# Kernel optimization log

Measured on AMD Instinct MI355X. Metric: run time of the kernel, lower is better.

## Reference

```python
import jax, jax.numpy as jnp
import numpy as np
from jax import lax

B = 4096
PRO_VOCAB, PRO_LEN, PRO_K = 25, 1000, 8
LIG_VOCAB, LIG_LEN, LIG_K = 64, 100, 4
CH = 96  # 2*CH = 192 = 6*32 per the reshape in the original forward
DN = ('NCH', 'OIH', 'NCH')  # 1D conv dimension numbers


def setup_inputs() -> dict:
    key = jax.random.key(0)
    ks = jax.random.split(key, 8)
    protein = jax.random.normal(ks[0], (B, PRO_VOCAB, PRO_LEN), dtype=jnp.float32)
    ligand = jax.random.normal(ks[1], (B, LIG_VOCAB, LIG_LEN), dtype=jnp.float32)
    w_pro = jax.random.normal(ks[2], (CH, PRO_VOCAB, PRO_K), dtype=jnp.float32) * 0.05
    b_pro = jnp.zeros((CH,), dtype=jnp.float32)
    w_lig = jax.random.normal(ks[3], (CH, LIG_VOCAB, LIG_K), dtype=jnp.float32) * 0.05
    b_lig = jnp.zeros((CH,), dtype=jnp.float32)
    # QuLinear readout over the 32*32=1024 amplitude-encoded Gram matrix -> scalar
    w_aff = jax.random.normal(ks[4], (1024,), dtype=jnp.float32) * 0.05
    b_aff = jnp.zeros((), dtype=jnp.float32)
    return {"protein": protein, "ligand": ligand, "w_pro": w_pro, "b_pro": b_pro,
            "w_lig": w_lig, "b_lig": b_lig, "w_aff": w_aff, "b_aff": b_aff}


def _conv_branch(x, w, b):
    # Conv1d (valid) -> ReLU -> global max pool over length  =>  (B, CH)
    y = lax.conv_general_dilated(x, w, (1,), 'VALID', dimension_numbers=DN)
    return jnp.max(jax.nn.relu(y + b[None, :, None]), axis=-1)


def reference(protein, ligand, w_pro, b_pro, w_lig, b_lig, w_aff, b_aff):
    x1 = _conv_branch(ligand, w_lig, b_lig)    # (B, 96)
    x2 = _conv_branch(protein, w_pro, b_pro)   # (B, 96)
    x = jnp.concatenate([x1, x2], axis=1).reshape(-1, 6, 32)  # (B, 6, 32)
    # Vectorized per-sample Gram matrix a.T @ a : (B, 32, 32)
    gram = jnp.einsum('bij,bik->bjk', x, x)
    flat = gram.reshape(gram.shape[0], -1)     # (B, 1024)
    # Amplitude encoding: L2-normalize the flattened Gram matrix per sample
    amp = flat / (jnp.linalg.norm(flat, axis=1, keepdims=True) + 1e-12)
    # QuLinear readout -> scalar affinity per sample
    aff = amp @ w_aff + b_aff                  # (B,)
    return aff
```

## Files before the change

kernel.cpp:

```cpp
#include <hip/hip_runtime.h>
#include <math.h>

typedef _Float16 f16;
typedef _Float16 f16x2 __attribute__((ext_vector_type(2)));
typedef _Float16 f16x4 __attribute__((ext_vector_type(4)));
typedef _Float16 f16x8 __attribute__((ext_vector_type(8)));
typedef float f32x4 __attribute__((ext_vector_type(4)));
typedef float f32x16 __attribute__((ext_vector_type(16)));

template<int V, int K, int VP>
__global__ void repack_kernel(const float* __restrict__ w, f16* __restrict__ wp) {
    int i = blockIdx.x * 256 + threadIdx.x;
    if (i >= K * 96 * VP) return;
    int v = i % VP, ch = (i / VP) % 96, t = i / (VP * 96);
    float val = (v < V) ? w[(ch * V + v) * K + t] : 0.f;
    wp[i] = (f16)val;
}

__global__ __launch_bounds__(256, 2) void conv_pro_kernel(
    const float* __restrict__ in,
    const f16*   __restrict__ wp,
    const float* __restrict__ bias,
    float* __restrict__ feat,
    int feat_off)
{
    constexpr int V = 25, L = 1000, KT = 8, LOUT = 993;
    constexpr int CH  = 256;
    constexpr int NC  = 4;
    constexpr int BR  = 264;
    constexpr int RSB = 80;
    constexpr int P4  = BR / 4;
    constexpr int NVP = 13;
    constexpr int NU  = NVP * P4;
    constexpr int NW  = KT * 96 * 32;

    __shared__ __align__(16) char s_raw[BR * RSB];
    __shared__ __align__(16) f16  s_w[NW];
    __shared__ float s_red[4 * 96];

    const int tid  = threadIdx.x;
    const int wave = tid >> 6;
    const int lane = tid & 63;
    const int g    = lane >> 4;
    const int r16  = lane & 15;
    const size_t b = blockIdx.x;
    const float* gs = in + b * (size_t)(V * L);

    {
        const f16x8* wg = (const f16x8*)wp;
        f16x8* wl = (f16x8*)s_w;
        #pragma unroll
        for (int u = 0; u < NW / 8 / 256; ++u)
            wl[u * 256 + tid] = wg[u * 256 + tid];
    }
    for (int row = tid; row < BR; row += 256) {
        const int swz = ((row >> 3) & 3) << 4;
        *(f16x8*)(s_raw + row * RSB + (48 ^ swz)) = (f16x8){};
    }
    __syncthreads();

    float runmax[6];
    #pragma unroll
    for (int c6 = 0; c6 < 6; ++c6) runmax[c6] = -3.0e38f;

    for (int c = 0; c < NC; ++c) {
        if (c) __syncthreads();
        #pragma unroll
        for (int u = 0; u < 4; ++u) {
            const int i = u * 256 + tid;
            if (i < NU) {
                const int v2 = i / P4, p4 = i - v2 * P4;
                const int p  = 4 * p4;
                const int gp = c * CH + p;
                float4 x0 = {0.f, 0.f, 0.f, 0.f}, x1 = {0.f, 0.f, 0.f, 0.f};
                if (gp < L) {
                    x0 = *(const float4*)(gs + (size_t)(2 * v2) * L + gp);
                    if (2 * v2 + 1 < V)
                        x1 = *(const float4*)(gs + (size_t)(2 * v2 + 1) * L + gp);
                }
                const int pb = 4 * v2;
                const int slot = pb & 48, sub = pb & 12;
                const float vx0[4] = {x0.x, x0.y, x0.z, x0.w};
                const float vx1[4] = {x1.x, x1.y, x1.z, x1.w};
                #pragma unroll
                for (int j = 0; j < 4; ++j) {
                    const int row = p + j;
                    const int swz = ((row >> 3) & 3) << 4;
                    f16x2 hv = { (f16)vx0[j], (f16)vx1[j] };
                    *(f16x2*)(s_raw + row * RSB + ((slot ^ swz) + sub)) = hv;
                }
            }
        }
        __syncthreads();

        f32x4 acc[4][6] = {};
        #pragma unroll 1
        for (int t = 0; t < KT; ++t) {
            f16x8 bf[6];
            #pragma unroll
            for (int c6 = 0; c6 < 6; ++c6)
                bf[c6] = *(const f16x8*)(s_w + (t * 96 + c6 * 16 + r16) * 32 + g * 8);
            #pragma unroll
            for (int rt = 0; rt < 4; ++rt) {
                const int row = wave * 64 + rt * 16 + r16 + t;
                const int swz = ((row >> 3) & 3) << 4;
                f16x8 a = *(const f16x8*)(s_raw + row * RSB + ((g * 16) ^ swz));
                #pragma unroll
                for (int c6 = 0; c6 < 6; ++c6)
                    acc[rt][c6] = __builtin_amdgcn_mfma_f32_16x16x32_f16(a, bf[c6], acc[rt][c6], 0, 0, 0);
            }
        }
        #pragma unroll
        for (int rt = 0; rt < 4; ++rt) {
            const int pt = c * CH + wave * 64 + rt * 16;
            if (pt + 16 <= LOUT) {
                #pragma unroll
                for (int c6 = 0; c6 < 6; ++c6)
                    #pragma unroll
                    for (int i = 0; i < 4; ++i)
                        runmax[c6] = fmaxf(runmax[c6], acc[rt][c6][i]);
            } else {
                const int p0g = pt + g * 4;
                #pragma unroll
                for (int c6 = 0; c6 < 6; ++c6)
                    #pragma unroll
                    for (int i = 0; i < 4; ++i)
                        if (p0g + i < LOUT) runmax[c6] = fmaxf(runmax[c6], acc[rt][c6][i]);
            }
        }
    }

    #pragma unroll
    for (int c6 = 0; c6 < 6; ++c6) {
        runmax[c6] = fmaxf(runmax[c6], __shfl_xor(runmax[c6], 16, 64));
        runmax[c6] = fmaxf(runmax[c6], __shfl_xor(runmax[c6], 32, 64));
    }
    if (lane < 16) {
        #pragma unroll
        for (int c6 = 0; c6 < 6; ++c6)
            s_red[wave * 96 + c6 * 16 + lane] = runmax[c6];
    }
    __syncthreads();
    if (tid < 96) {
        float m = fmaxf(fmaxf(s_red[tid], s_red[96 + tid]),
                        fmaxf(s_red[192 + tid], s_red[288 + tid]));
        feat[b * 192 + feat_off + tid] = fmaxf(m + bias[tid], 0.f);
    }
}

__global__ __launch_bounds__(384) void conv_lig_kernel(
    const float* __restrict__ in,
    const f16*   __restrict__ wp,
    const float* __restrict__ bias,
    float* __restrict__ feat,
    int feat_off)
{
    constexpr int V = 64, L = 100, KT = 4, VP = 64, KSTEPS = 4;
    constexpr int LP = 132, RS = 72, NTILES = 4, LOUT = 97;
    constexpr int RSB = RS * 2, NQ = V / 4;
    __shared__ __align__(16) char s_raw[LP * RSB];

    const int tid  = threadIdx.x;
    const int b    = blockIdx.x;
    const int wave = tid >> 6;
    const int lane = tid & 63;
    const int colw = wave % 3;
    const int roww = wave / 3;
    const int q    = lane >> 5;
    const int r    = lane & 31;

    {
        float4 z = {0.f, 0.f, 0.f, 0.f};
        float4* sz = (float4*)s_raw;
        for (int i = tid; i < LP * RSB / 16; i += 384) sz[i] = z;
    }
    __syncthreads();

    const float* gin = in + (size_t)b * (V * L);
    for (int i = tid; i < NQ * L; i += 384) {
        int q4 = i / L, p = i - q4 * L;
        const float* gp = gin + q4 * 4 * L + p;
        f16x4 hv = { (f16)gp[0], (f16)gp[L], (f16)gp[2 * L], (f16)gp[3 * L] };
        int off = (8 * q4) ^ (((p >> 3) & 3) << 4);
        *(f16x4*)(s_raw + p * RSB + off) = hv;
    }

    f16x8 bfr[KT][KSTEPS];
    #pragma unroll
    for (int t = 0; t < KT; ++t)
        #pragma unroll
        for (int ks = 0; ks < KSTEPS; ++ks)
            bfr[t][ks] = *(const f16x8*)(wp + (t * 96 + colw * 32 + r) * VP + ks * 16 + q * 8);

    __syncthreads();

    float runmax = -3.0e38f;
    for (int it = 0; it < NTILES / 2; ++it) {
        const int p0 = (roww * (NTILES / 2) + it) * 32;
        f32x16 acc = {};
        #pragma unroll
        for (int t = 0; t < KT; ++t) {
            int row = p0 + r + t;
            if (row > LP - 1) row = LP - 1;
            const char* ap = s_raw + row * RSB;
            const int swz = ((row >> 3) & 3) << 4;
            #pragma unroll
            for (int ks = 0; ks < KSTEPS; ++ks) {
                f16x8 af = *(const f16x8*)(ap + ((ks * 32 + q * 16) ^ swz));
                acc = __builtin_amdgcn_mfma_f32_32x32x16_f16(af, bfr[t][ks], acc, 0, 0, 0);
            }
        }
        #pragma unroll
        for (int i = 0; i < 16; ++i) {
            int rr = (i & 3) + 8 * (i >> 2) + 4 * q;
            if (p0 + rr < LOUT) runmax = fmaxf(runmax, acc[i]);
        }
    }
    runmax = fmaxf(runmax, __shfl_xor(runmax, 32, 64));

    __syncthreads();
    float* s_red = (float*)s_raw;
    if (lane < 32) s_red[roww * 96 + colw * 32 + r] = runmax;
    __syncthreads();
    if (tid < 96) {
        float m = fmaxf(s_red[tid], s_red[96 + tid]);
        feat[(size_t)b * 192 + feat_off + tid] = fmaxf(m + bias[tid], 0.f);
    }
}

__global__ __launch_bounds__(256) void gram_affinity_kernel(
    const float* __restrict__ feat, const float* __restrict__ w_aff,
    const float* __restrict__ b_aff, float* __restrict__ out, int B)
{
    const int lane = threadIdx.x & 63;
    const int wid  = threadIdx.x >> 6;
    const int b    = blockIdx.x * 4 + wid;

    __shared__ float s_x[4][192];

    if (b < B) {
        const float* fp = feat + (size_t)b * 192;
        for (int i = lane; i < 192; i += 64) s_x[wid][i] = fp[i];
    }
    __syncthreads();

    if (b < B) {
        float ssum = 0.f, sdot = 0.f;
        #pragma unroll
        for (int t = 0; t < 16; ++t) {
            const int jk = t * 64 + lane;
            const int j = jk >> 5, k = jk & 31;
            float gg = 0.f;
            #pragma unroll
            for (int i = 0; i < 6; ++i)
                gg = fmaf(s_x[wid][i * 32 + j], s_x[wid][i * 32 + k], gg);
            ssum = fmaf(gg, gg, ssum);
            sdot = fmaf(gg, w_aff[jk], sdot);
        }
        #pragma unroll
        for (int off = 32; off >= 1; off >>= 1) {
            ssum += __shfl_xor(ssum, off, 64);
            sdot += __shfl_xor(sdot, off, 64);
        }
        if (lane == 0) out[b] = sdot / (sqrtf(ssum) + 1e-12f) + b_aff[0];
    }
}

extern "C" void kernel_launch(void* const* d_in, const int* in_sizes, int n_in,
                              void* d_out, int out_size, void* d_ws, size_t ws_size,
                              hipStream_t stream)
{
    const float* protein = (const float*)d_in[0];
    const float* ligand  = (const float*)d_in[1];
    const float* w_pro   = (const float*)d_in[2];
    const float* b_pro   = (const float*)d_in[3];
    const float* w_lig   = (const float*)d_in[4];
    const float* b_lig   = (const float*)d_in[5];
    const float* w_aff   = (const float*)d_in[6];
    const float* b_aff   = (const float*)d_in[7];
    float* out = (float*)d_out;
    const int B = out_size;

    float* feat   = (float*)d_ws;
    f16*   wpackP = (f16*)((char*)d_ws + (size_t)B * 192 * 4);
    f16*   wpackL = wpackP + 8 * 96 * 32;

    repack_kernel<25, 8, 32><<<96, 256, 0, stream>>>(w_pro, wpackP);
    repack_kernel<64, 4, 64><<<96, 256, 0, stream>>>(w_lig, wpackL);

    conv_lig_kernel<<<B, 384, 0, stream>>>(ligand, wpackL, b_lig, feat, 0);
    conv_pro_kernel<<<B, 256, 0, stream>>>(protein, wpackP, b_pro, feat, 96);

    gram_affinity_kernel<<<(B + 3) / 4, 256, 0, stream>>>(feat, w_aff, b_aff, out, B);
}
```

Baseline: 304.2 us.

## Fuse Gram affinity readout into protein conv kernel with double-buffered 512-thread staging

The protein conv kernel now runs 512 threads per sample, processes the sequence in two 512-row chunks with double-buffered LDS, and overlaps staging of the second chunk with MFMA compute on the first. Staging writes 8 channels per 16-byte store using a new XOR swizzle. The Gram matrix plus normalized readout is folded into the kernel's epilogue, which removes the separate gram kernel launch and the feature round trip. The cost is larger LDS use (about 83 KB, one block per CU) and a serialized epilogue inside each block.

```diff
diff --git a/kernel.cpp b/kernel.cpp
--- a/kernel.cpp
+++ b/kernel.cpp
@@ -2,7 +2,6 @@
 #include <math.h>
 
 typedef _Float16 f16;
-typedef _Float16 f16x2 __attribute__((ext_vector_type(2)));
 typedef _Float16 f16x4 __attribute__((ext_vector_type(4)));
 typedef _Float16 f16x8 __attribute__((ext_vector_type(8)));
 typedef float f32x4 __attribute__((ext_vector_type(4)));
@@ -17,26 +16,28 @@
     wp[i] = (f16)val;
 }
 
-__global__ __launch_bounds__(256, 2) void conv_pro_kernel(
+__global__ __launch_bounds__(512, 1) void conv_pro_fused_kernel(
     const float* __restrict__ in,
     const f16*   __restrict__ wp,
     const float* __restrict__ bias,
-    float* __restrict__ feat,
-    int feat_off)
+    const float* __restrict__ feat_lig,
+    const float* __restrict__ w_aff,
+    const float* __restrict__ b_aff,
+    float* __restrict__ out)
 {
     constexpr int V = 25, L = 1000, KT = 8, LOUT = 993;
-    constexpr int CH  = 256;
-    constexpr int NC  = 4;
-    constexpr int BR  = 264;
+    constexpr int CH  = 512;
+    constexpr int NC  = 2;
+    constexpr int BR  = 520;
     constexpr int RSB = 80;
     constexpr int P4  = BR / 4;
-    constexpr int NVP = 13;
-    constexpr int NU  = NVP * P4;
+    constexpr int NU  = 4 * P4;
     constexpr int NW  = KT * 96 * 32;
 
-    __shared__ __align__(16) char s_raw[BR * RSB];
+    __shared__ __align__(16) char s_buf[2][BR * RSB];
     __shared__ __align__(16) f16  s_w[NW];
-    __shared__ float s_red[4 * 96];
+    __shared__ float s_red[8 * 96];
+    __shared__ float s_x[192];
 
     const int tid  = threadIdx.x;
     const int wave = tid >> 6;
@@ -46,53 +47,38 @@
     const size_t b = blockIdx.x;
     const float* gs = in + b * (size_t)(V * L);
 
-    {
-        const f16x8* wg = (const f16x8*)wp;
-        f16x8* wl = (f16x8*)s_w;
-        #pragma unroll
-        for (int u = 0; u < NW / 8 / 256; ++u)
-            wl[u * 256 + tid] = wg[u * 256 + tid];
-    }
-    for (int row = tid; row < BR; row += 256) {
-        const int swz = ((row >> 3) & 3) << 4;
-        *(f16x8*)(s_raw + row * RSB + (48 ^ swz)) = (f16x8){};
-    }
-    __syncthreads();
+    auto SWZ = [](int row) { return (((row >> 3) ^ (row >> 5)) & 3) << 4; };
+
+    auto stage = [&](int c, char* sb) {
+        const int base = c * CH;
+        for (int i = tid; i < NU; i += 512) {
+            const int vg = i / P4, p4 = i - vg * P4;
+            const int p = 4 * p4, gp = base + p;
+            float x[8][4];
+            #pragma unroll
+            for (int vv = 0; vv < 8; ++vv) {
+                const int v = vg * 8 + vv;
+                float4 t4 = {0.f, 0.f, 0.f, 0.f};
+                if (gp < L && v < V)
+                    t4 = *(const float4*)(gs + (size_t)v * L + gp);
+                x[vv][0] = t4.x; x[vv][1] = t4.y; x[vv][2] = t4.z; x[vv][3] = t4.w;
+            }
+            #pragma unroll
+            for (int j = 0; j < 4; ++j) {
+                const int row = p + j;
+                f16x8 hv;
+                #pragma unroll
+                for (int vv = 0; vv < 8; ++vv) hv[vv] = (f16)x[vv][j];
+                *(f16x8*)(sb + row * RSB + ((vg * 16) ^ SWZ(row))) = hv;
+            }
+        }
+    };
 
     float runmax[6];
     #pragma unroll
     for (int c6 = 0; c6 < 6; ++c6) runmax[c6] = -3.0e38f;
 
-    for (int c = 0; c < NC; ++c) {
-        if (c) __syncthreads();
-        #pragma unroll
-        for (int u = 0; u < 4; ++u) {
-            const int i = u * 256 + tid;
-            if (i < NU) {
-                const int v2 = i / P4, p4 = i - v2 * P4;
-                const int p  = 4 * p4;
-                const int gp = c * CH + p;
-                float4 x0 = {0.f, 0.f, 0.f, 0.f}, x1 = {0.f, 0.f, 0.f, 0.f};
-                if (gp < L) {
-                    x0 = *(const float4*)(gs + (size_t)(2 * v2) * L + gp);
-                    if (2 * v2 + 1 < V)
-                        x1 = *(const float4*)(gs + (size_t)(2 * v2 + 1) * L + gp);
-                }
-                const int pb = 4 * v2;
-                const int slot = pb & 48, sub = pb & 12;
-                const float vx0[4] = {x0.x, x0.y, x0.z, x0.w};
-                const float vx1[4] = {x1.x, x1.y, x1.z, x1.w};
-                #pragma unroll
-                for (int j = 0; j < 4; ++j) {
-                    const int row = p + j;
-                    const int swz = ((row >> 3) & 3) << 4;
-                    f16x2 hv = { (f16)vx0[j], (f16)vx1[j] };
-                    *(f16x2*)(s_raw + row * RSB + ((slot ^ swz) + sub)) = hv;
-                }
-            }
-        }
-        __syncthreads();
-
+    auto compute = [&](int c, const char* sb) {
         f32x4 acc[4][6] = {};
         #pragma unroll 1
         for (int t = 0; t < KT; ++t) {
@@ -101,34 +87,48 @@
             for (int c6 = 0; c6 < 6; ++c6)
                 bf[c6] = *(const f16x8*)(s_w + (t * 96 + c6 * 16 + r16) * 32 + g * 8);
             #pragma unroll
-            for (int rt = 0; rt < 4; ++rt) {
-                const int row = wave * 64 + rt * 16 + r16 + t;
-                const int swz = ((row >> 3) & 3) << 4;
-                f16x8 a = *(const f16x8*)(s_raw + row * RSB + ((g * 16) ^ swz));
+            for (int tt = 0; tt < 4; ++tt) {
+                const int row = (wave * 4 + tt) * 16 + r16 + t;
+                f16x8 a = *(const f16x8*)(sb + row * RSB + ((g * 16) ^ SWZ(row)));
                 #pragma unroll
                 for (int c6 = 0; c6 < 6; ++c6)
-                    acc[rt][c6] = __builtin_amdgcn_mfma_f32_16x16x32_f16(a, bf[c6], acc[rt][c6], 0, 0, 0);
-            }
-        }
-        #pragma unroll
-        for (int rt = 0; rt < 4; ++rt) {
-            const int pt = c * CH + wave * 64 + rt * 16;
+                    acc[tt][c6] = __builtin_amdgcn_mfma_f32_16x16x32_f16(a, bf[c6], acc[tt][c6], 0, 0, 0);
+            }
+        }
+        #pragma unroll
+        for (int tt = 0; tt < 4; ++tt) {
+            const int pt = c * CH + (wave * 4 + tt) * 16;
             if (pt + 16 <= LOUT) {
                 #pragma unroll
                 for (int c6 = 0; c6 < 6; ++c6)
                     #pragma unroll
                     for (int i = 0; i < 4; ++i)
-                        runmax[c6] = fmaxf(runmax[c6], acc[rt][c6][i]);
+                        runmax[c6] = fmaxf(runmax[c6], acc[tt][c6][i]);
             } else {
                 const int p0g = pt + g * 4;
                 #pragma unroll
                 for (int c6 = 0; c6 < 6; ++c6)
                     #pragma unroll
                     for (int i = 0; i < 4; ++i)
-                        if (p0g + i < LOUT) runmax[c6] = fmaxf(runmax[c6], acc[rt][c6][i]);
-            }
-        }
-    }
+                        if (p0g + i < LOUT) runmax[c6] = fmaxf(runmax[c6], acc[tt][c6][i]);
+            }
+        }
+    };
+
+    {
+        const f16x8* wg = (const f16x8*)wp;
+        f16x8* wl = (f16x8*)s_w;
+        #pragma unroll
+        for (int u = 0; u < NW / 8 / 512; ++u)
+            wl[u * 512 + tid] = wg[u * 512 + tid];
+    }
+    stage(0, s_buf[0]);
+    __syncthreads();
+
+    stage(1, s_buf[1]);
+    compute(0, s_buf[0]);
+    __syncthreads();
+    compute(1, s_buf[1]);
 
     #pragma unroll
     for (int c6 = 0; c6 < 6; ++c6) {
@@ -141,10 +141,40 @@
             s_red[wave * 96 + c6 * 16 + lane] = runmax[c6];
     }
     __syncthreads();
+
     if (tid < 96) {
-        float m = fmaxf(fmaxf(s_red[tid], s_red[96 + tid]),
-                        fmaxf(s_red[192 + tid], s_red[288 + tid]));
-        feat[b * 192 + feat_off + tid] = fmaxf(m + bias[tid], 0.f);
+        float m = s_red[tid];
+        #pragma unroll
+        for (int w = 1; w < 8; ++w) m = fmaxf(m, s_red[w * 96 + tid]);
+        s_x[96 + tid] = fmaxf(m + bias[tid], 0.f);
+        s_x[tid] = feat_lig[b * 192 + tid];
+    }
+    __syncthreads();
+
+    float ssum = 0.f, sdot = 0.f;
+    #pragma unroll
+    for (int u = 0; u < 2; ++u) {
+        const int jk = u * 512 + tid;
+        const int j = jk >> 5, k = jk & 31;
+        float gg = 0.f;
+        #pragma unroll
+        for (int i = 0; i < 6; ++i)
+            gg = fmaf(s_x[i * 32 + j], s_x[i * 32 + k], gg);
+        ssum = fmaf(gg, gg, ssum);
+        sdot = fmaf(gg, w_aff[jk], sdot);
+    }
+    #pragma unroll
+    for (int off = 32; off >= 1; off >>= 1) {
+        ssum += __shfl_xor(ssum, off, 64);
+        sdot += __shfl_xor(sdot, off, 64);
+    }
+    if (lane == 0) { s_red[wave] = ssum; s_red[8 + wave] = sdot; }
+    __syncthreads();
+    if (tid == 0) {
+        float S = 0.f, D = 0.f;
+        #pragma unroll
+        for (int w = 0; w < 8; ++w) { S += s_red[w]; D += s_red[8 + w]; }
+        out[b] = D / (sqrtf(S) + 1e-12f) + b_aff[0];
     }
 }
 
@@ -225,44 +255,6 @@
     if (tid < 96) {
         float m = fmaxf(s_red[tid], s_red[96 + tid]);
         feat[(size_t)b * 192 + feat_off + tid] = fmaxf(m + bias[tid], 0.f);
-    }
-}
-
-__global__ __launch_bounds__(256) void gram_affinity_kernel(
-    const float* __restrict__ feat, const float* __restrict__ w_aff,
-    const float* __restrict__ b_aff, float* __restrict__ out, int B)
-{
-    const int lane = threadIdx.x & 63;
-    const int wid  = threadIdx.x >> 6;
-    const int b    = blockIdx.x * 4 + wid;
-
-    __shared__ float s_x[4][192];
-
-    if (b < B) {
-        const float* fp = feat + (size_t)b * 192;
-        for (int i = lane; i < 192; i += 64) s_x[wid][i] = fp[i];
-    }
-    __syncthreads();
-
-    if (b < B) {
-        float ssum = 0.f, sdot = 0.f;
-        #pragma unroll
-        for (int t = 0; t < 16; ++t) {
-            const int jk = t * 64 + lane;
-            const int j = jk >> 5, k = jk & 31;
-            float gg = 0.f;
-            #pragma unroll
-            for (int i = 0; i < 6; ++i)
-                gg = fmaf(s_x[wid][i * 32 + j], s_x[wid][i * 32 + k], gg);
-            ssum = fmaf(gg, gg, ssum);
-            sdot = fmaf(gg, w_aff[jk], sdot);
-        }
-        #pragma unroll
-        for (int off = 32; off >= 1; off >>= 1) {
-            ssum += __shfl_xor(ssum, off, 64);
-            sdot += __shfl_xor(sdot, off, 64);
-        }
-        if (lane == 0) out[b] = sdot / (sqrtf(ssum) + 1e-12f) + b_aff[0];
     }
 }
 
@@ -289,7 +281,6 @@
     repack_kernel<64, 4, 64><<<96, 256, 0, stream>>>(w_lig, wpackL);
 
     conv_lig_kernel<<<B, 384, 0, stream>>>(ligand, wpackL, b_lig, feat, 0);
-    conv_pro_kernel<<<B, 256, 0, stream>>>(protein, wpackP, b_pro, feat, 96);
-
-    gram_affinity_kernel<<<(B + 3) / 4, 256, 0, stream>>>(feat, w_aff, b_aff, out, B);
-}
+    conv_pro_fused_kernel<<<B, 512, 0, stream>>>(
+        protein, wpackP, b_pro, feat, w_aff, b_aff, out);
+}
```

Result: slower. 402.1 us (+32.2%).

## Repack protein conv weights per lane and write input staging as f16x8 rows

Applied to the files above, without the earlier changes.

Protein weights are now repacked in per-lane MFMA fragment order, so each B-fragment load from shared memory is contiguous per lane. The input staging loop has each thread load 8 vocab channels for 4 positions and write one f16x8 per row, replacing many 2-element f16 stores. It also uses a new XOR swizzle that mixes row bits 3 and 5, and drops the explicit zeroing of the pad slot because padded vocab entries are now written as zeros. The aim is fewer LDS store instructions and fewer bank conflicts, at the cost of more registers per thread during staging.

```diff
diff --git a/kernel.cpp b/kernel.cpp
--- a/kernel.cpp
+++ b/kernel.cpp
@@ -2,7 +2,6 @@
 #include <math.h>
 
 typedef _Float16 f16;
-typedef _Float16 f16x2 __attribute__((ext_vector_type(2)));
 typedef _Float16 f16x4 __attribute__((ext_vector_type(4)));
 typedef _Float16 f16x8 __attribute__((ext_vector_type(8)));
 typedef float f32x4 __attribute__((ext_vector_type(4)));
@@ -13,6 +12,17 @@
     int i = blockIdx.x * 256 + threadIdx.x;
     if (i >= K * 96 * VP) return;
     int v = i % VP, ch = (i / VP) % 96, t = i / (VP * 96);
+    float val = (v < V) ? w[(ch * V + v) * K + t] : 0.f;
+    wp[i] = (f16)val;
+}
+
+__global__ void repack_pro_kernel(const float* __restrict__ w, f16* __restrict__ wp) {
+    constexpr int V = 25, K = 8;
+    int i = blockIdx.x * 256 + threadIdx.x;
+    if (i >= K * 6 * 64 * 8) return;
+    int e = i & 7, l = (i >> 3) & 63, c6 = (i >> 9) % 6, t = i / (512 * 6);
+    int r16 = l & 15, g = l >> 4;
+    int ch = c6 * 16 + r16, v = g * 8 + e;
     float val = (v < V) ? w[(ch * V + v) * K + t] : 0.f;
     wp[i] = (f16)val;
 }
@@ -30,9 +40,8 @@
     constexpr int BR  = 264;
     constexpr int RSB = 80;
     constexpr int P4  = BR / 4;
-    constexpr int NVP = 13;
-    constexpr int NU  = NVP * P4;
-    constexpr int NW  = KT * 96 * 32;
+    constexpr int NU  = 4 * P4;
+    constexpr int NW  = KT * 6 * 64 * 8;
 
     __shared__ __align__(16) char s_raw[BR * RSB];
     __shared__ __align__(16) f16  s_w[NW];
@@ -46,6 +55,8 @@
     const size_t b = blockIdx.x;
     const float* gs = in + b * (size_t)(V * L);
 
+    auto SWZ = [](int row) { return (((row >> 3) ^ (row >> 5)) & 3) << 4; };
+
     {
         const f16x8* wg = (const f16x8*)wp;
         f16x8* wl = (f16x8*)s_w;
@@ -53,10 +64,6 @@
         for (int u = 0; u < NW / 8 / 256; ++u)
             wl[u * 256 + tid] = wg[u * 256 + tid];
     }
-    for (int row = tid; row < BR; row += 256) {
-        const int swz = ((row >> 3) & 3) << 4;
-        *(f16x8*)(s_raw + row * RSB + (48 ^ swz)) = (f16x8){};
-    }
     __syncthreads();
 
     float runmax[6];
@@ -66,28 +73,27 @@
     for (int c = 0; c < NC; ++c) {
         if (c) __syncthreads();
         #pragma unroll
-        for (int u = 0; u < 4; ++u) {
+        for (int u = 0; u < 2; ++u) {
             const int i = u * 256 + tid;
             if (i < NU) {
-                const int v2 = i / P4, p4 = i - v2 * P4;
-                const int p  = 4 * p4;
-                const int gp = c * CH + p;
-                float4 x0 = {0.f, 0.f, 0.f, 0.f}, x1 = {0.f, 0.f, 0.f, 0.f};
-                if (gp < L) {
-                    x0 = *(const float4*)(gs + (size_t)(2 * v2) * L + gp);
-                    if (2 * v2 + 1 < V)
-                        x1 = *(const float4*)(gs + (size_t)(2 * v2 + 1) * L + gp);
+                const int vg = i / P4, p4 = i - vg * P4;
+                const int p = 4 * p4, gp = c * CH + p;
+                float x[8][4];
+                #pragma unroll
+                for (int vv = 0; vv < 8; ++vv) {
+                    const int v = vg * 8 + vv;
+                    float4 t4 = {0.f, 0.f, 0.f, 0.f};
+                    if (gp < L && v < V)
+                        t4 = *(const float4*)(gs + (size_t)v * L + gp);
+                    x[vv][0] = t4.x; x[vv][1] = t4.y; x[vv][2] = t4.z; x[vv][3] = t4.w;
                 }
-                const int pb = 4 * v2;
-                const int slot = pb & 48, sub = pb & 12;
-                const float vx0[4] = {x0.x, x0.y, x0.z, x0.w};
-                const float vx1[4] = {x1.x, x1.y, x1.z, x1.w};
                 #pragma unroll
                 for (int j = 0; j < 4; ++j) {
                     const int row = p + j;
-                    const int swz = ((row >> 3) & 3) << 4;
-                    f16x2 hv = { (f16)vx0[j], (f16)vx1[j] };
-                    *(f16x2*)(s_raw + row * RSB + ((slot ^ swz) + sub)) = hv;
+                    f16x8 hv;
+                    #pragma unroll
+                    for (int vv = 0; vv < 8; ++vv) hv[vv] = (f16)x[vv][j];
+                    *(f16x8*)(s_raw + row * RSB + ((vg * 16) ^ SWZ(row))) = hv;
                 }
             }
         }
@@ -99,33 +105,32 @@
             f16x8 bf[6];
             #pragma unroll
             for (int c6 = 0; c6 < 6; ++c6)
-                bf[c6] = *(const f16x8*)(s_w + (t * 96 + c6 * 16 + r16) * 32 + g * 8);
+                bf[c6] = *(const f16x8*)(s_w + ((t * 6 + c6) * 64 + lane) * 8);
             #pragma unroll
-            for (int rt = 0; rt < 4; ++rt) {
-                const int row = wave * 64 + rt * 16 + r16 + t;
-                const int swz = ((row >> 3) & 3) << 4;
-                f16x8 a = *(const f16x8*)(s_raw + row * RSB + ((g * 16) ^ swz));
+            for (int tt = 0; tt < 4; ++tt) {
+                const int row = (wave * 4 + tt) * 16 + r16 + t;
+                f16x8 a = *(const f16x8*)(s_raw + row * RSB + ((g * 16) ^ SWZ(row)));
                 #pragma unroll
                 for (int c6 = 0; c6 < 6; ++c6)
-                    acc[rt][c6] = __builtin_amdgcn_mfma_f32_16x16x32_f16(a, bf[c6], acc[rt][c6], 0, 0, 0);
+                    acc[tt][c6] = __builtin_amdgcn_mfma_f32_16x16x32_f16(a, bf[c6], acc[tt][c6], 0, 0, 0);
             }
         }
         #pragma unroll
-        for (int rt = 0; rt < 4; ++rt) {
-            const int pt = c * CH + wave * 64 + rt * 16;
+        for (int tt = 0; tt < 4; ++tt) {
+            const int pt = c * CH + (wave * 4 + tt) * 16;
             if (pt + 16 <= LOUT) {
                 #pragma unroll
                 for (int c6 = 0; c6 < 6; ++c6)
                     #pragma unroll
                     for (int i = 0; i < 4; ++i)
-                        runmax[c6] = fmaxf(runmax[c6], acc[rt][c6][i]);
+                        runmax[c6] = fmaxf(runmax[c6], acc[tt][c6][i]);
             } else {
                 const int p0g = pt + g * 4;
                 #pragma unroll
                 for (int c6 = 0; c6 < 6; ++c6)
                     #pragma unroll
                     for (int i = 0; i < 4; ++i)
-                        if (p0g + i < LOUT) runmax[c6] = fmaxf(runmax[c6], acc[rt][c6][i]);
+                        if (p0g + i < LOUT) runmax[c6] = fmaxf(runmax[c6], acc[tt][c6][i]);
             }
         }
     }
@@ -283,9 +288,9 @@
 
     float* feat   = (float*)d_ws;
     f16*   wpackP = (f16*)((char*)d_ws + (size_t)B * 192 * 4);
-    f16*   wpackL = wpackP + 8 * 96 * 32;
-
-    repack_kernel<25, 8, 32><<<96, 256, 0, stream>>>(w_pro, wpackP);
+    f16*   wpackL = wpackP + 24576;
+
+    repack_pro_kernel<<<96, 256, 0, stream>>>(w_pro, wpackP);
     repack_kernel<64, 4, 64><<<96, 256, 0, stream>>>(w_lig, wpackL);
 
     conv_lig_kernel<<<B, 384, 0, stream>>>(ligand, wpackL, b_lig, feat, 0);
```

Measured after the change: 359.2 us. +18.0%, slower.
